# Performance work log

Hardware: AMD Instinct MI355X
Metric: run time of the kernel (lower is better)

Reference implementation:

```python
import jax, jax.numpy as jnp
import numpy as np

B, S, D = 1, 2048, 4096
NH, NKV, HD = 32, 8, 128
N_REP = NH // NKV
NEG = -1e9


def setup_inputs() -> dict:
    key = jax.random.key(0)
    ks = jax.random.split(key, 8)
    x = jax.random.normal(ks[0], (B, S, D), dtype=jnp.float32)
    # rotary freqs (theta=10000), shape [S, HD//2]
    inv = 1.0 / (10000.0 ** (jnp.arange(0, HD, 2, dtype=jnp.float32) / HD))
    ang = jnp.arange(S, dtype=jnp.float32)[:, None] * inv[None, :]
    freqs_cos, freqs_sin = jnp.cos(ang), jnp.sin(ang)
    # causal mask [1,1,S,S]
    row = jnp.arange(S)[:, None]
    col = jnp.arange(S)[None, :]
    mask = jnp.where(col <= row, 0.0, NEG).astype(jnp.float32)[None, None]
    input_indexes = jnp.arange(S, dtype=jnp.int64)
    cache_k = jnp.zeros((B, S, NKV, HD), dtype=jnp.float32)
    cache_v = jnp.zeros((B, S, NKV, HD), dtype=jnp.float32)
    sc = 0.02
    wq = jax.random.normal(ks[1], (NH * HD, D), dtype=jnp.float32) * sc
    wk = jax.random.normal(ks[2], (NKV * HD, D), dtype=jnp.float32) * sc
    wv = jax.random.normal(ks[3], (NKV * HD, D), dtype=jnp.float32) * sc
    wo = jax.random.normal(ks[4], (NH * HD, D), dtype=jnp.float32).T * sc
    return {"x": x, "freqs_cos": freqs_cos, "freqs_sin": freqs_sin, "mask": mask,
            "input_indexes": input_indexes, "cache_k": cache_k, "cache_v": cache_v,
            "wq": wq, "wk": wk, "wv": wv, "wo": wo}


def _rope(t, cos, sin):
    # t: [B,S,H,HD]; treat last dim as HD//2 complex pairs (even=real, odd=imag)
    tr = t.reshape(*t.shape[:-1], HD // 2, 2)
    xr, xi = tr[..., 0], tr[..., 1]
    c = cos[None, :, None, :]  # [1,S,1,HD//2]
    s = sin[None, :, None, :]
    outr = xr * c - xi * s
    outi = xr * s + xi * c
    return jnp.stack([outr, outi], axis=-1).reshape(t.shape)


def reference(x, freqs_cos, freqs_sin, mask, input_indexes, cache_k, cache_v, wq, wk, wv, wo):
    bsz, seqlen = x.shape[0], x.shape[-2]
    xq = (x @ wq.T).reshape(bsz, seqlen, NH, HD)
    xk = (x @ wk.T).reshape(bsz, seqlen, NKV, HD)
    xv = (x @ wv.T).reshape(bsz, seqlen, NKV, HD)
    xq = _rope(xq, freqs_cos, freqs_sin)
    xk = _rope(xk, freqs_cos, freqs_sin)
    # KV-cache append (index_copy along seq dim)
    cache_k = cache_k.at[:, input_indexes].set(xk)
    cache_v = cache_v.at[:, input_indexes].set(xv)
    # GQA: repeat kv heads
    keys = jnp.repeat(cache_k, N_REP, axis=2)    # [B,S,NH,HD]
    values = jnp.repeat(cache_v, N_REP, axis=2)
    scores = jnp.einsum('bshd,bthd->bhst', xq, keys) / jnp.sqrt(jnp.float32(HD))
    scores = scores + mask
    probs = jax.nn.softmax(scores.astype(jnp.float32), axis=-1).astype(xq.dtype)
    out = jnp.einsum('bhst,bthd->bhsd', probs, values)
    out = out.transpose(0, 2, 1, 3).reshape(bsz, seqlen, -1)
    return (out @ wo.T, cache_k, cache_v)
```

## Files before the change

kernel.cpp:

```cpp
#include <hip/hip_runtime.h>
#include <cstdint>

#define S_LEN 2048
#define D_DIM 4096
#define NH_ 32
#define NKV_ 8
#define HD_ 128
#define GK 4096

typedef unsigned short u16;
typedef __attribute__((ext_vector_type(4))) float f32x4;
typedef __attribute__((ext_vector_type(8))) short bf16x8;
typedef __attribute__((ext_vector_type(4))) short s16x4;

__device__ __forceinline__ short f2bf(float f) {
  union { float f; unsigned int u; } v; v.f = f;
  unsigned int r = v.u + 0x7fffu + ((v.u >> 16) & 1u);
  return (short)(r >> 16);
}

__device__ __forceinline__ void glds16(const void* g, void* l) {
  __builtin_amdgcn_global_load_lds(
      (const __attribute__((address_space(1))) void*)g,
      (__attribute__((address_space(3))) void*)l, 16, 0, 0);
}

__global__ __launch_bounds__(256) void cvt_bf16(const float* __restrict__ src,
                                                u16* __restrict__ dst, int n8) {
  int i = blockIdx.x * 256 + threadIdx.x;
  if (i < n8) {
    float4 a = *(const float4*)&src[(size_t)i * 8];
    float4 b = *(const float4*)&src[(size_t)i * 8 + 4];
    bf16x8 o = { f2bf(a.x), f2bf(a.y), f2bf(a.z), f2bf(a.w),
                 f2bf(b.x), f2bf(b.y), f2bf(b.z), f2bf(b.w) };
    *(bf16x8*)&dst[(size_t)i * 8] = o;
  }
}

template <int MODE>
__global__ __launch_bounds__(256) void gemm_bf(const u16* __restrict__ A,
                                               const u16* __restrict__ W,
                                               float* __restrict__ C,
                                               u16* __restrict__ qbf,
                                               u16* __restrict__ kbf,
                                               u16* __restrict__ vbf,
                                               float* __restrict__ cko,
                                               float* __restrict__ cvo,
                                               const float* __restrict__ fc,
                                               const float* __restrict__ fs,
                                               int N) {
  __shared__ __align__(16) u16 As[128 * 64];
  __shared__ __align__(16) u16 Bs[128 * 64];
  const int t = threadIdx.x;
  const int lane = t & 63;
  const int wave = t >> 6;
  const int wm = (wave >> 1) * 64;
  const int wn = (wave & 1) * 64;
  const int quad = lane >> 4;
  const int L = lane & 15;
  const int bm = blockIdx.y * 128;
  const int bn = blockIdx.x * 128;
  const int dr = lane >> 3;
  const int cb = lane & 7;
  const int cbs = cb ^ dr;

  f32x4 acc[4][4];
#pragma unroll
  for (int i = 0; i < 4; ++i)
#pragma unroll
    for (int j = 0; j < 4; ++j) { f32x4 z = {0.f, 0.f, 0.f, 0.f}; acc[i][j] = z; }

  for (int k0 = 0; k0 < GK; k0 += 64) {
    __syncthreads();
#pragma unroll
    for (int q = 0; q < 4; ++q) {
      int chunk = wave * 4 + q;
      int row = chunk * 8 + dr;
      glds16(&A[(size_t)(bm + row) * GK + k0 + cbs * 8], &As[chunk * 512]);
      glds16(&W[(size_t)(bn + row) * GK + k0 + cbs * 8], &Bs[chunk * 512]);
    }
    __syncthreads();
#pragma unroll
    for (int s = 0; s < 2; ++s) {
      bf16x8 af[4], bw[4];
#pragma unroll
      for (int i = 0; i < 4; ++i)
        af[i] = *(const bf16x8*)&As[(wm + 16 * i + L) * 64 + (((s * 4 + quad) ^ (L & 7)) * 8)];
#pragma unroll
      for (int j = 0; j < 4; ++j)
        bw[j] = *(const bf16x8*)&Bs[(wn + 16 * j + L) * 64 + (((s * 4 + quad) ^ (L & 7)) * 8)];
#pragma unroll
      for (int i = 0; i < 4; ++i)
#pragma unroll
        for (int j = 0; j < 4; ++j)
          acc[i][j] = __builtin_amdgcn_mfma_f32_16x16x32_bf16(af[i], bw[j], acc[i][j], 0, 0, 0);
    }
  }

  if (MODE == 0) {
#pragma unroll
    for (int i = 0; i < 4; ++i) {
      int r0 = bm + wm + i * 16 + quad * 4;
#pragma unroll
      for (int j = 0; j < 4; ++j) {
        int c = bn + wn + j * 16 + L;
#pragma unroll
        for (int r = 0; r < 4; ++r) C[(size_t)(r0 + r) * N + c] = acc[i][j][r];
      }
    }
  } else {
    const float scale = 0.08838834764831845f;
#pragma unroll
    for (int i = 0; i < 4; ++i) {
#pragma unroll
      for (int j = 0; j < 4; ++j) {
        int c = bn + wn + 16 * j + L;
#pragma unroll
        for (int r = 0; r < 4; ++r) {
          int srow = bm + wm + 16 * i + 4 * quad + r;
          float v = acc[i][j][r];
          float partner = __shfl_xor(v, 1);
          if (c < 4096) {
            int p = (c >> 1) & 63;
            float co = fc[srow * 64 + p], si = fs[srow * 64 + p];
            float out = (c & 1) ? partner * si + v * co : v * co - partner * si;
            qbf[(size_t)srow * 4096 + c] = (u16)f2bf(out * scale);
          } else if (c < 5120) {
            int p = (c >> 1) & 63;
            float co = fc[srow * 64 + p], si = fs[srow * 64 + p];
            float out = (c & 1) ? partner * si + v * co : v * co - partner * si;
            int cc = c - 4096;
            cko[(size_t)srow * 1024 + cc] = out;
            kbf[(size_t)srow * 1024 + cc] = (u16)f2bf(out);
          } else {
            int cc = c - 5120;
            cvo[(size_t)srow * 1024 + cc] = v;
            vbf[(size_t)srow * 1024 + cc] = (u16)f2bf(v);
          }
        }
      }
    }
  }
}

__global__ __launch_bounds__(256, 3) void attn_bf(const u16* __restrict__ qbf,
                                                  const u16* __restrict__ kbf,
                                                  const u16* __restrict__ vbf,
                                                  u16* __restrict__ ao) {
  __shared__ __align__(16) u16 Ks[64 * 136];
  __shared__ __align__(16) u16 Vt[128 * 64];
  __shared__ __align__(16) u16 Ps[4 * 16 * 72];
  const int t = threadIdx.x;
  const int wave = t >> 6;
  const int lane = t & 63;
  const int Q4 = lane >> 4;
  const int L = lane & 15;
  const int h = blockIdx.y;
  const int qb = 31 - (int)blockIdx.x;
  const int kvh = h >> 2;
  const int qs0 = qb * 64;
  u16* Psw = &Ps[wave * 16 * 72];

  bf16x8 qf[4];
  {
    const u16* qbase = &qbf[(size_t)(qs0 + 16 * wave + L) * D_DIM + h * HD_ + 8 * Q4];
#pragma unroll
    for (int s = 0; s < 4; ++s) qf[s] = *(const bf16x8*)&qbase[32 * s];
  }

  f32x4 o[8];
#pragma unroll
  for (int jd = 0; jd < 8; ++jd) { f32x4 z = {0.f, 0.f, 0.f, 0.f}; o[jd] = z; }
  float mold[4] = {-1e30f, -1e30f, -1e30f, -1e30f};
  float lst[4] = {0.f, 0.f, 0.f, 0.f};

  for (int kt = 0; kt <= qb; ++kt) {
    __syncthreads();
    const u16* kb = &kbf[(size_t)(kt * 64) * (NKV_ * HD_) + kvh * HD_];
    const u16* vb = &vbf[(size_t)(kt * 64) * (NKV_ * HD_) + kvh * HD_];
#pragma unroll
    for (int p = 0; p < 4; ++p) {
      int u = t + 256 * p;
      int r = u >> 4, c8 = u & 15;
      *(bf16x8*)&Ks[r * 136 + c8 * 8] =
          *(const bf16x8*)&kb[(size_t)r * (NKV_ * HD_) + c8 * 8];
    }
#pragma unroll
    for (int p = 0; p < 4; ++p) {
      int u = t + 256 * p;
      int d = u & 127, bb = u >> 7;
      const u16* vsrc = &vb[(size_t)(bb * 8) * (NKV_ * HD_) + d];
      short vv[8];
#pragma unroll
      for (int j = 0; j < 8; ++j) vv[j] = (short)vsrc[(size_t)j * (NKV_ * HD_)];
      bf16x8 pk = { vv[0], vv[1], vv[2], vv[3], vv[4], vv[5], vv[6], vv[7] };
      *(bf16x8*)&Vt[d * 64 + ((bb + d) & 7) * 8] = pk;
    }
    __syncthreads();

    f32x4 sa[4];
#pragma unroll
    for (int jn = 0; jn < 4; ++jn) { f32x4 z = {0.f, 0.f, 0.f, 0.f}; sa[jn] = z; }
#pragma unroll
    for (int s = 0; s < 4; ++s) {
#pragma unroll
      for (int jn = 0; jn < 4; ++jn) {
        bf16x8 kf = *(const bf16x8*)&Ks[(16 * jn + L) * 136 + 32 * s + 8 * Q4];
        sa[jn] = __builtin_amdgcn_mfma_f32_16x16x32_bf16(qf[s], kf, sa[jn], 0, 0, 0);
      }
    }

    const int gq0 = qs0 + 16 * wave + 4 * Q4;
    const int gk0 = kt * 64 + L;
    float rmax[4];
#pragma unroll
    for (int r = 0; r < 4; ++r) {
#pragma unroll
      for (int jn = 0; jn < 4; ++jn)
        if (gk0 + 16 * jn > gq0 + r) sa[jn][r] = -1e30f;
      rmax[r] = fmaxf(fmaxf(sa[0][r], sa[1][r]), fmaxf(sa[2][r], sa[3][r]));
    }
#pragma unroll
    for (int m = 1; m < 16; m <<= 1) {
#pragma unroll
      for (int r = 0; r < 4; ++r) rmax[r] = fmaxf(rmax[r], __shfl_xor(rmax[r], m));
    }
    float p_[4][4], rsum[4], alpha[4];
#pragma unroll
    for (int r = 0; r < 4; ++r) {
      float mnew = fmaxf(mold[r], rmax[r]);
      alpha[r] = __expf(mold[r] - mnew);
#pragma unroll
      for (int jn = 0; jn < 4; ++jn) p_[jn][r] = __expf(sa[jn][r] - mnew);
      rsum[r] = (p_[0][r] + p_[1][r]) + (p_[2][r] + p_[3][r]);
      mold[r] = mnew;
    }
#pragma unroll
    for (int m = 1; m < 16; m <<= 1) {
#pragma unroll
      for (int r = 0; r < 4; ++r) rsum[r] += __shfl_xor(rsum[r], m);
    }
#pragma unroll
    for (int r = 0; r < 4; ++r) lst[r] = lst[r] * alpha[r] + rsum[r];
#pragma unroll
    for (int jd = 0; jd < 8; ++jd)
#pragma unroll
      for (int r = 0; r < 4; ++r) o[jd][r] *= alpha[r];

#pragma unroll
    for (int r = 0; r < 4; ++r)
#pragma unroll
      for (int jn = 0; jn < 4; ++jn)
        Psw[(4 * Q4 + r) * 72 + 16 * jn + L] = (u16)f2bf(p_[jn][r]);
    asm volatile("s_waitcnt lgkmcnt(0)" ::: "memory");

#pragma unroll
    for (int s2 = 0; s2 < 2; ++s2) {
      bf16x8 pa = *(const bf16x8*)&Psw[L * 72 + 32 * s2 + 8 * Q4];
#pragma unroll
      for (int jd = 0; jd < 8; ++jd) {
        bf16x8 vf = *(const bf16x8*)&Vt[(16 * jd + L) * 64 + ((4 * s2 + Q4 + L) & 7) * 8];
        o[jd] = __builtin_amdgcn_mfma_f32_16x16x32_bf16(pa, vf, o[jd], 0, 0, 0);
      }
    }
  }

  float inv[4];
#pragma unroll
  for (int r = 0; r < 4; ++r) inv[r] = 1.0f / lst[r];
#pragma unroll
  for (int r = 0; r < 4; ++r) {
    u16* dst = &ao[(size_t)(qs0 + 16 * wave + 4 * Q4 + r) * D_DIM + h * HD_ + L];
#pragma unroll
    for (int jd = 0; jd < 8; ++jd) dst[16 * jd] = (u16)f2bf(o[jd][r] * inv[r]);
  }
}

#define LDA 40
__global__ __launch_bounds__(256) void gemm_bt(const float* __restrict__ A,
                                               const float* __restrict__ W,
                                               float* __restrict__ C, int N) {
  __shared__ short As[128 * LDA];
  __shared__ short Bs[128 * LDA];
  const int t = threadIdx.x;
  const int lane = t & 63;
  const int wave = t >> 6;
  const int wm = (wave >> 1) * 64;
  const int wn = (wave & 1) * 64;
  const int quad = lane >> 4;
  const int l15 = lane & 15;
  const int bm = blockIdx.y * 128;
  const int bn = blockIdx.x * 128;
  f32x4 acc[4][4];
#pragma unroll
  for (int i = 0; i < 4; ++i)
#pragma unroll
    for (int j = 0; j < 4; ++j) { f32x4 z = {0.f, 0.f, 0.f, 0.f}; acc[i][j] = z; }
  for (int k0 = 0; k0 < GK; k0 += 32) {
    __syncthreads();
#pragma unroll
    for (int p = 0; p < 4; ++p) {
      int idx = p * 256 + t;
      int row = idx >> 3;
      int c4 = (idx & 7) * 4;
      const float4 av = *(const float4*)&A[(size_t)(bm + row) * GK + k0 + c4];
      const float4 wv = *(const float4*)&W[(size_t)(bn + row) * GK + k0 + c4];
      s16x4 a4 = { f2bf(av.x), f2bf(av.y), f2bf(av.z), f2bf(av.w) };
      s16x4 w4 = { f2bf(wv.x), f2bf(wv.y), f2bf(wv.z), f2bf(wv.w) };
      *(s16x4*)&As[row * LDA + c4] = a4;
      *(s16x4*)&Bs[row * LDA + c4] = w4;
    }
    __syncthreads();
    bf16x8 af[4], bfr[4];
#pragma unroll
    for (int i = 0; i < 4; ++i) {
      af[i]  = *(const bf16x8*)&As[(wm + i * 16 + l15) * LDA + quad * 8];
      bfr[i] = *(const bf16x8*)&Bs[(wn + i * 16 + l15) * LDA + quad * 8];
    }
#pragma unroll
    for (int i = 0; i < 4; ++i)
#pragma unroll
      for (int j = 0; j < 4; ++j)
        acc[i][j] = __builtin_amdgcn_mfma_f32_16x16x32_bf16(af[i], bfr[j], acc[i][j], 0, 0, 0);
  }
#pragma unroll
  for (int i = 0; i < 4; ++i) {
    int r0 = bm + wm + i * 16 + quad * 4;
#pragma unroll
    for (int j = 0; j < 4; ++j) {
      int c = bn + wn + j * 16 + l15;
#pragma unroll
      for (int r = 0; r < 4; ++r) C[(size_t)(r0 + r) * N + c] = acc[i][j][r];
    }
  }
}

__global__ __launch_bounds__(256) void rope_kernel(float* __restrict__ xq,
                                                   const float* __restrict__ xk,
                                                   float* __restrict__ cko,
                                                   const float* __restrict__ fc,
                                                   const float* __restrict__ fs) {
  int i = blockIdx.x * 256 + threadIdx.x;
  const int NQP = S_LEN * NH_ * (HD_ / 2);
  if (i < NQP) {
    int s = i >> 11; int rem = i & 2047; int p = rem & 63;
    float c = fc[s * 64 + p], sn = fs[s * 64 + p];
    float2 v = *(const float2*)&xq[(size_t)s * D_DIM + 2 * rem];
    *(float2*)&xq[(size_t)s * D_DIM + 2 * rem] =
        make_float2(v.x * c - v.y * sn, v.x * sn + v.y * c);
  } else {
    int j = i - NQP; int s = j >> 9; int rem = j & 511; int p = rem & 63;
    float c = fc[s * 64 + p], sn = fs[s * 64 + p];
    float2 v = *(const float2*)&xk[(size_t)s * (NKV_ * HD_) + 2 * rem];
    *(float2*)&cko[(size_t)s * (NKV_ * HD_) + 2 * rem] =
        make_float2(v.x * c - v.y * sn, v.x * sn + v.y * c);
  }
}

__global__ __launch_bounds__(256, 3) void attn_mfma(const float* __restrict__ xq,
                                                    const float* __restrict__ ck,
                                                    const float* __restrict__ cv,
                                                    float* __restrict__ outp) {
  __shared__ __align__(16) short Ks[64 * 136];
  __shared__ __align__(16) short Vt[128 * 64];
  __shared__ __align__(16) short Ps[4 * 16 * 72];
  const int t = threadIdx.x;
  const int wave = t >> 6;
  const int lane = t & 63;
  const int Q4 = lane >> 4;
  const int L = lane & 15;
  const int h = blockIdx.y;
  const int qb = 31 - (int)blockIdx.x;
  const int kvh = h >> 2;
  const int qs0 = qb * 64;
  const float scale = 0.08838834764831845f;
  short* Psw = &Ps[wave * 16 * 72];
  bf16x8 qf[4];
  {
    const float* qbase = &xq[(size_t)(qs0 + 16 * wave + L) * D_DIM + h * HD_ + 8 * Q4];
#pragma unroll
    for (int s = 0; s < 4; ++s) {
      float4 a = *(const float4*)&qbase[32 * s];
      float4 b = *(const float4*)&qbase[32 * s + 4];
      bf16x8 q8 = { f2bf(a.x * scale), f2bf(a.y * scale), f2bf(a.z * scale), f2bf(a.w * scale),
                    f2bf(b.x * scale), f2bf(b.y * scale), f2bf(b.z * scale), f2bf(b.w * scale) };
      qf[s] = q8;
    }
  }
  f32x4 o[8];
#pragma unroll
  for (int jd = 0; jd < 8; ++jd) { f32x4 z = {0.f, 0.f, 0.f, 0.f}; o[jd] = z; }
  float mold[4] = {-1e30f, -1e30f, -1e30f, -1e30f};
  float lst[4] = {0.f, 0.f, 0.f, 0.f};
  for (int kt = 0; kt <= qb; ++kt) {
    __syncthreads();
    const float* ckb = &ck[(size_t)(kt * 64) * (NKV_ * HD_) + kvh * HD_];
    const float* cvb = &cv[(size_t)(kt * 64) * (NKV_ * HD_) + kvh * HD_];
#pragma unroll
    for (int p = 0; p < 8; ++p) {
      int i = t + 256 * p;
      int r = i >> 5, c4 = (i & 31) * 4;
      float4 v = *(const float4*)&ckb[(size_t)r * (NKV_ * HD_) + c4];
      s16x4 k4 = { f2bf(v.x), f2bf(v.y), f2bf(v.z), f2bf(v.w) };
      *(s16x4*)&Ks[r * 136 + c4] = k4;
    }
#pragma unroll
    for (int p = 0; p < 4; ++p) {
      int u = t + 256 * p;
      int d = u & 127, bb = u >> 7;
      float vv[8];
#pragma unroll
      for (int j = 0; j < 8; ++j) vv[j] = cvb[(size_t)(bb * 8 + j) * (NKV_ * HD_) + d];
      bf16x8 pk = { f2bf(vv[0]), f2bf(vv[1]), f2bf(vv[2]), f2bf(vv[3]),
                    f2bf(vv[4]), f2bf(vv[5]), f2bf(vv[6]), f2bf(vv[7]) };
      *(bf16x8*)&Vt[d * 64 + ((bb + d) & 7) * 8] = pk;
    }
    __syncthreads();
    f32x4 sa[4];
#pragma unroll
    for (int jn = 0; jn < 4; ++jn) { f32x4 z = {0.f, 0.f, 0.f, 0.f}; sa[jn] = z; }
#pragma unroll
    for (int s = 0; s < 4; ++s) {
#pragma unroll
      for (int jn = 0; jn < 4; ++jn) {
        bf16x8 kf = *(const bf16x8*)&Ks[(16 * jn + L) * 136 + 32 * s + 8 * Q4];
        sa[jn] = __builtin_amdgcn_mfma_f32_16x16x32_bf16(qf[s], kf, sa[jn], 0, 0, 0);
      }
    }
    const int gq0 = qs0 + 16 * wave + 4 * Q4;
    const int gk0 = kt * 64 + L;
    float rmax[4];
#pragma unroll
    for (int r = 0; r < 4; ++r) {
#pragma unroll
      for (int jn = 0; jn < 4; ++jn)
        if (gk0 + 16 * jn > gq0 + r) sa[jn][r] = -1e30f;
      rmax[r] = fmaxf(fmaxf(sa[0][r], sa[1][r]), fmaxf(sa[2][r], sa[3][r]));
    }
#pragma unroll
    for (int m = 1; m < 16; m <<= 1) {
#pragma unroll
      for (int r = 0; r < 4; ++r) rmax[r] = fmaxf(rmax[r], __shfl_xor(rmax[r], m));
    }
    float p_[4][4], rsum[4], alpha[4];
#pragma unroll
    for (int r = 0; r < 4; ++r) {
      float mnew = fmaxf(mold[r], rmax[r]);
      alpha[r] = __expf(mold[r] - mnew);
#pragma unroll
      for (int jn = 0; jn < 4; ++jn) p_[jn][r] = __expf(sa[jn][r] - mnew);
      rsum[r] = (p_[0][r] + p_[1][r]) + (p_[2][r] + p_[3][r]);
      mold[r] = mnew;
    }
#pragma unroll
    for (int m = 1; m < 16; m <<= 1) {
#pragma unroll
      for (int r = 0; r < 4; ++r) rsum[r] += __shfl_xor(rsum[r], m);
    }
#pragma unroll
    for (int r = 0; r < 4; ++r) lst[r] = lst[r] * alpha[r] + rsum[r];
#pragma unroll
    for (int jd = 0; jd < 8; ++jd)
#pragma unroll
      for (int r = 0; r < 4; ++r) o[jd][r] *= alpha[r];
#pragma unroll
    for (int r = 0; r < 4; ++r)
#pragma unroll
      for (int jn = 0; jn < 4; ++jn)
        Psw[(4 * Q4 + r) * 72 + 16 * jn + L] = f2bf(p_[jn][r]);
    asm volatile("s_waitcnt lgkmcnt(0)" ::: "memory");
#pragma unroll
    for (int s2 = 0; s2 < 2; ++s2) {
      bf16x8 pa = *(const bf16x8*)&Psw[L * 72 + 32 * s2 + 8 * Q4];
#pragma unroll
      for (int jd = 0; jd < 8; ++jd) {
        bf16x8 vf = *(const bf16x8*)&Vt[(16 * jd + L) * 64 + ((4 * s2 + Q4 + L) & 7) * 8];
        o[jd] = __builtin_amdgcn_mfma_f32_16x16x32_bf16(pa, vf, o[jd], 0, 0, 0);
      }
    }
  }
  float inv[4];
#pragma unroll
  for (int r = 0; r < 4; ++r) inv[r] = 1.0f / lst[r];
#pragma unroll
  for (int r = 0; r < 4; ++r) {
    float* dst = &outp[(size_t)(qs0 + 16 * wave + 4 * Q4 + r) * D_DIM + h * HD_ + L];
#pragma unroll
    for (int jd = 0; jd < 8; ++jd) dst[16 * jd] = o[jd][r] * inv[r];
  }
}

extern "C" void kernel_launch(void* const* d_in, const int* in_sizes, int n_in,
                              void* d_out, int out_size, void* d_ws, size_t ws_size,
                              hipStream_t stream) {
  (void)in_sizes; (void)n_in; (void)out_size;
  const float* x  = (const float*)d_in[0];
  const float* fc = (const float*)d_in[1];
  const float* fs = (const float*)d_in[2];
  const float* wq = (const float*)d_in[7];
  const float* wk = (const float*)d_in[8];
  const float* wv = (const float*)d_in[9];
  const float* wo = (const float*)d_in[10];
  float* outp = (float*)d_out;
  float* ck = outp + (size_t)S_LEN * D_DIM;
  float* cv = ck + (size_t)S_LEN * NKV_ * HD_;

  if (ws_size >= 109051904ull) {
    u16* x_bf = (u16*)d_ws;
    u16* wqkv = x_bf + 8388608;
    u16* q_bf = wqkv + 25165824;
    u16* k_bf = q_bf + 8388608;
    u16* v_bf = k_bf + 2097152;
    u16* ao_bf = v_bf + 2097152;
    u16* wo_bf = wqkv;

    cvt_bf16<<<4096, 256, 0, stream>>>(x, x_bf, 1048576);
    cvt_bf16<<<8192, 256, 0, stream>>>(wq, wqkv, 2097152);
    cvt_bf16<<<2048, 256, 0, stream>>>(wk, wqkv + 16777216, 524288);
    cvt_bf16<<<2048, 256, 0, stream>>>(wv, wqkv + 20971520, 524288);
    gemm_bf<1><<<dim3(48, 16), 256, 0, stream>>>(x_bf, wqkv, nullptr, q_bf,
                                                 k_bf, v_bf, ck, cv, fc, fs, 6144);
    cvt_bf16<<<8192, 256, 0, stream>>>(wo, wo_bf, 2097152);
    attn_bf<<<dim3(32, 32), 256, 0, stream>>>(q_bf, k_bf, v_bf, ao_bf);
    gemm_bf<0><<<dim3(32, 16), 256, 0, stream>>>(ao_bf, wo_bf, outp, nullptr,
                                                 nullptr, nullptr, nullptr,
                                                 nullptr, fc, fs, 4096);
  } else {
    float* xq = (float*)d_ws;
    float* xk = xq + (size_t)S_LEN * D_DIM;
    dim3 blk(256);
    gemm_bt<<<dim3(32, 16), blk, 0, stream>>>(x, wq, xq, 4096);
    gemm_bt<<<dim3(8, 16),  blk, 0, stream>>>(x, wk, xk, 1024);
    gemm_bt<<<dim3(8, 16),  blk, 0, stream>>>(x, wv, cv, 1024);
    rope_kernel<<<20480, 256, 0, stream>>>(xq, xk, ck, fc, fs);
    attn_mfma<<<dim3(32, 32), 512 / 2, 0, stream>>>(xq, ck, cv, xq);
    gemm_bt<<<dim3(32, 16), blk, 0, stream>>>(xq, wo, outp, 4096);
  }
}
```

Baseline: 650.6 us.

## Replace bf16 GEMM with 256x256 tile, 8-wave, double-buffered pipelined kernel

Swaps the 128x128 single-buffered GEMM for a 256x256 tile kernel with 8 waves and double-buffered LDS. Global-to-LDS loads are issued in quarter stages and interleaved with MFMA phases, with explicit vmcnt and lgkmcnt waits, barriers and priority raises. The goal is to hide load latency and raise operand reuse per block. In exchange the grid gets much smaller (192 and 128 blocks on 256 CUs), so some CUs may sit idle, and register pressure rises.

```diff
diff --git a/kernel.cpp b/kernel.cpp
--- a/kernel.cpp
+++ b/kernel.cpp
@@ -38,87 +38,173 @@
 }
 
 template <int MODE>
-__global__ __launch_bounds__(256) void gemm_bf(const u16* __restrict__ A,
-                                               const u16* __restrict__ W,
-                                               float* __restrict__ C,
-                                               u16* __restrict__ qbf,
-                                               u16* __restrict__ kbf,
-                                               u16* __restrict__ vbf,
-                                               float* __restrict__ cko,
-                                               float* __restrict__ cvo,
-                                               const float* __restrict__ fc,
-                                               const float* __restrict__ fs,
-                                               int N) {
-  __shared__ __align__(16) u16 As[128 * 64];
-  __shared__ __align__(16) u16 Bs[128 * 64];
+__global__ __launch_bounds__(512, 1) void gemm8(const u16* __restrict__ Amat,
+                                                const u16* __restrict__ W,
+                                                float* __restrict__ C,
+                                                u16* __restrict__ qbf,
+                                                u16* __restrict__ kbf,
+                                                u16* __restrict__ vbf,
+                                                float* __restrict__ cko,
+                                                float* __restrict__ cvo,
+                                                const float* __restrict__ fc,
+                                                const float* __restrict__ fs,
+                                                int N) {
+  __shared__ __align__(16) u16 As[2][16384];
+  __shared__ __align__(16) u16 Bs[2][16384];
   const int t = threadIdx.x;
   const int lane = t & 63;
   const int wave = t >> 6;
-  const int wm = (wave >> 1) * 64;
-  const int wn = (wave & 1) * 64;
+  const int wr = wave >> 2;
+  const int wc = wave & 3;
   const int quad = lane >> 4;
   const int L = lane & 15;
-  const int bm = blockIdx.y * 128;
-  const int bn = blockIdx.x * 128;
+  const int bm = blockIdx.y * 256;
+  const int bn = blockIdx.x * 256;
   const int dr = lane >> 3;
   const int cb = lane & 7;
   const int cbs = cb ^ dr;
-
-  f32x4 acc[4][4];
-#pragma unroll
-  for (int i = 0; i < 4; ++i)
+  const int NT = GK / 64;
+
+  auto stage = [&](int s) {
+    const int tile = s >> 2;
+    const int p = s & 3;
+    const int half = p & 1;
+    const int buf = tile & 1;
+    const int k0 = tile << 6;
+    const bool isB = (p < 2);
+    const u16* src = isB ? W : Amat;
+    const int base = isB ? bn : bm;
+    u16* dst = isB ? &Bs[buf][0] : &As[buf][0];
+    const int chunk0 = half * 16 + wave * 2;
+#pragma unroll
+    for (int c = 0; c < 2; ++c) {
+      const int chunk = chunk0 + c;
+      const int row = chunk * 8 + dr;
+      glds16(&src[(size_t)(base + row) * GK + k0 + cbs * 8], &dst[chunk * 512]);
+    }
+  };
+
+  f32x4 acc[8][4];
+#pragma unroll
+  for (int i = 0; i < 8; ++i)
 #pragma unroll
     for (int j = 0; j < 4; ++j) { f32x4 z = {0.f, 0.f, 0.f, 0.f}; acc[i][j] = z; }
 
-  for (int k0 = 0; k0 < GK; k0 += 64) {
-    __syncthreads();
-#pragma unroll
-    for (int q = 0; q < 4; ++q) {
-      int chunk = wave * 4 + q;
-      int row = chunk * 8 + dr;
-      glds16(&A[(size_t)(bm + row) * GK + k0 + cbs * 8], &As[chunk * 512]);
-      glds16(&W[(size_t)(bn + row) * GK + k0 + cbs * 8], &Bs[chunk * 512]);
-    }
-    __syncthreads();
-#pragma unroll
-    for (int s = 0; s < 2; ++s) {
-      bf16x8 af[4], bw[4];
-#pragma unroll
-      for (int i = 0; i < 4; ++i)
-        af[i] = *(const bf16x8*)&As[(wm + 16 * i + L) * 64 + (((s * 4 + quad) ^ (L & 7)) * 8)];
-#pragma unroll
-      for (int j = 0; j < 4; ++j)
-        bw[j] = *(const bf16x8*)&Bs[(wn + 16 * j + L) * 64 + (((s * 4 + quad) ^ (L & 7)) * 8)];
-#pragma unroll
-      for (int i = 0; i < 4; ++i)
-#pragma unroll
-        for (int j = 0; j < 4; ++j)
-          acc[i][j] = __builtin_amdgcn_mfma_f32_16x16x32_bf16(af[i], bw[j], acc[i][j], 0, 0, 0);
-    }
+  stage(0); stage(1); stage(2); stage(3);
+  asm volatile("s_waitcnt vmcnt(4)" ::: "memory");
+  stage(4); stage(5); stage(6);
+  asm volatile("s_waitcnt vmcnt(6)" ::: "memory");
+  __builtin_amdgcn_s_barrier();
+  __builtin_amdgcn_sched_barrier(0);
+
+  bf16x8 af[4][2], bw[4][2];
+  const int arow = wr * 128;
+  const int brow = wc * 64;
+
+  for (int kt = 0; kt < NT; ++kt) {
+    const u16* as = &As[kt & 1][0];
+    const u16* bs = &Bs[kt & 1][0];
+#pragma unroll
+    for (int i = 0; i < 4; ++i)
+#pragma unroll
+      for (int k = 0; k < 2; ++k)
+        af[i][k] = *(const bf16x8*)&as[(arow + i * 16 + L) * 64 +
+                                       (((k * 4 + quad) ^ (L & 7)) * 8)];
+#pragma unroll
+    for (int j = 0; j < 4; ++j)
+#pragma unroll
+      for (int k = 0; k < 2; ++k)
+        bw[j][k] = *(const bf16x8*)&bs[(brow + j * 16 + L) * 64 +
+                                       (((k * 4 + quad) ^ (L & 7)) * 8)];
+    { int s = 4 * kt + 7; if (s < 4 * NT) stage(s); }
+    __builtin_amdgcn_s_barrier();
+    asm volatile("s_waitcnt lgkmcnt(0)" ::: "memory");
+    __builtin_amdgcn_sched_barrier(0);
+    __builtin_amdgcn_s_setprio(1);
+#pragma unroll
+    for (int i = 0; i < 4; ++i)
+#pragma unroll
+      for (int j = 0; j < 2; ++j)
+#pragma unroll
+        for (int k = 0; k < 2; ++k)
+          acc[i][j] = __builtin_amdgcn_mfma_f32_16x16x32_bf16(af[i][k], bw[j][k],
+                                                              acc[i][j], 0, 0, 0);
+    __builtin_amdgcn_s_setprio(0);
+    __builtin_amdgcn_s_barrier();
+    { int s = 4 * kt + 8; if (s < 4 * NT) stage(s); }
+    __builtin_amdgcn_s_barrier();
+    __builtin_amdgcn_s_setprio(1);
+#pragma unroll
+    for (int i = 0; i < 4; ++i)
+#pragma unroll
+      for (int j = 0; j < 2; ++j)
+#pragma unroll
+        for (int k = 0; k < 2; ++k)
+          acc[i][2 + j] = __builtin_amdgcn_mfma_f32_16x16x32_bf16(
+              af[i][k], bw[2 + j][k], acc[i][2 + j], 0, 0, 0);
+    __builtin_amdgcn_s_setprio(0);
+    __builtin_amdgcn_s_barrier();
+#pragma unroll
+    for (int i = 0; i < 4; ++i)
+#pragma unroll
+      for (int k = 0; k < 2; ++k)
+        af[i][k] = *(const bf16x8*)&as[(arow + 64 + i * 16 + L) * 64 +
+                                       (((k * 4 + quad) ^ (L & 7)) * 8)];
+    { int s = 4 * kt + 9; if (s < 4 * NT) stage(s); }
+    __builtin_amdgcn_s_barrier();
+    asm volatile("s_waitcnt lgkmcnt(0)" ::: "memory");
+    __builtin_amdgcn_sched_barrier(0);
+    __builtin_amdgcn_s_setprio(1);
+#pragma unroll
+    for (int i = 0; i < 4; ++i)
+#pragma unroll
+      for (int j = 0; j < 2; ++j)
+#pragma unroll
+        for (int k = 0; k < 2; ++k)
+          acc[4 + i][j] = __builtin_amdgcn_mfma_f32_16x16x32_bf16(
+              af[i][k], bw[j][k], acc[4 + i][j], 0, 0, 0);
+    __builtin_amdgcn_s_setprio(0);
+    __builtin_amdgcn_s_barrier();
+    { int s = 4 * kt + 10; if (s < 4 * NT) stage(s); }
+    __builtin_amdgcn_s_barrier();
+    __builtin_amdgcn_s_setprio(1);
+#pragma unroll
+    for (int i = 0; i < 4; ++i)
+#pragma unroll
+      for (int j = 0; j < 2; ++j)
+#pragma unroll
+        for (int k = 0; k < 2; ++k)
+          acc[4 + i][2 + j] = __builtin_amdgcn_mfma_f32_16x16x32_bf16(
+              af[i][k], bw[2 + j][k], acc[4 + i][2 + j], 0, 0, 0);
+    __builtin_amdgcn_s_setprio(0);
+    if (kt + 2 < NT) asm volatile("s_waitcnt vmcnt(6)" ::: "memory");
+    else             asm volatile("s_waitcnt vmcnt(0)" ::: "memory");
+    __builtin_amdgcn_s_barrier();
+    __builtin_amdgcn_sched_barrier(0);
   }
 
   if (MODE == 0) {
 #pragma unroll
-    for (int i = 0; i < 4; ++i) {
-      int r0 = bm + wm + i * 16 + quad * 4;
-#pragma unroll
-      for (int j = 0; j < 4; ++j) {
-        int c = bn + wn + j * 16 + L;
-#pragma unroll
-        for (int r = 0; r < 4; ++r) C[(size_t)(r0 + r) * N + c] = acc[i][j][r];
+    for (int mi = 0; mi < 8; ++mi) {
+      int r0 = bm + wr * 128 + mi * 16 + quad * 4;
+#pragma unroll
+      for (int ni = 0; ni < 4; ++ni) {
+        int c = bn + wc * 64 + ni * 16 + L;
+#pragma unroll
+        for (int r = 0; r < 4; ++r) C[(size_t)(r0 + r) * N + c] = acc[mi][ni][r];
       }
     }
   } else {
     const float scale = 0.08838834764831845f;
 #pragma unroll
-    for (int i = 0; i < 4; ++i) {
-#pragma unroll
-      for (int j = 0; j < 4; ++j) {
-        int c = bn + wn + 16 * j + L;
+    for (int mi = 0; mi < 8; ++mi) {
+#pragma unroll
+      for (int ni = 0; ni < 4; ++ni) {
+        int c = bn + wc * 64 + ni * 16 + L;
 #pragma unroll
         for (int r = 0; r < 4; ++r) {
-          int srow = bm + wm + 16 * i + 4 * quad + r;
-          float v = acc[i][j][r];
+          int srow = bm + wr * 128 + mi * 16 + 4 * quad + r;
+          float v = acc[mi][ni][r];
           float partner = __shfl_xor(v, 1);
           if (c < 4096) {
             int p = (c >> 1) & 63;
@@ -518,13 +604,13 @@
     cvt_bf16<<<8192, 256, 0, stream>>>(wq, wqkv, 2097152);
     cvt_bf16<<<2048, 256, 0, stream>>>(wk, wqkv + 16777216, 524288);
     cvt_bf16<<<2048, 256, 0, stream>>>(wv, wqkv + 20971520, 524288);
-    gemm_bf<1><<<dim3(48, 16), 256, 0, stream>>>(x_bf, wqkv, nullptr, q_bf,
-                                                 k_bf, v_bf, ck, cv, fc, fs, 6144);
+    gemm8<1><<<dim3(24, 8), 512, 0, stream>>>(x_bf, wqkv, nullptr, q_bf,
+                                              k_bf, v_bf, ck, cv, fc, fs, 6144);
     cvt_bf16<<<8192, 256, 0, stream>>>(wo, wo_bf, 2097152);
     attn_bf<<<dim3(32, 32), 256, 0, stream>>>(q_bf, k_bf, v_bf, ao_bf);
-    gemm_bf<0><<<dim3(32, 16), 256, 0, stream>>>(ao_bf, wo_bf, outp, nullptr,
-                                                 nullptr, nullptr, nullptr,
-                                                 nullptr, fc, fs, 4096);
+    gemm8<0><<<dim3(16, 8), 512, 0, stream>>>(ao_bf, wo_bf, outp, nullptr,
+                                              nullptr, nullptr, nullptr,
+                                              nullptr, fc, fs, 4096);
   } else {
     float* xq = (float*)d_ws;
     float* xk = xq + (size_t)S_LEN * D_DIM;
```

Result: slower. 684.4 us (+5.2%).

## Use 256x256 double-buffered GEMM tiles and 128-row attention blocks

Applied to the files above, without the earlier changes.

Replaces the 128x128 bf16 GEMM with a 512-thread kernel that computes 256x256 output tiles. It double-buffers LDS with staggered A/B prefetch, manual waitcnt/barrier scheduling and s_setprio around the MFMA bursts. The attention kernel moves to 512 threads handling 128 query rows per block, which halves redundant K/V tile loads per head. The larger tiles shrink the grids (192 and 128 GEMM blocks, 512 attention blocks), which may leave compute units idle on a large GPU. The attention change also relies on the unshown causal-masking code handling the new tile count.

```diff
diff --git a/kernel.cpp b/kernel.cpp
--- a/kernel.cpp
+++ b/kernel.cpp
@@ -38,87 +38,130 @@
 }
 
 template <int MODE>
-__global__ __launch_bounds__(256) void gemm_bf(const u16* __restrict__ A,
-                                               const u16* __restrict__ W,
-                                               float* __restrict__ C,
-                                               u16* __restrict__ qbf,
-                                               u16* __restrict__ kbf,
-                                               u16* __restrict__ vbf,
-                                               float* __restrict__ cko,
-                                               float* __restrict__ cvo,
-                                               const float* __restrict__ fc,
-                                               const float* __restrict__ fs,
-                                               int N) {
-  __shared__ __align__(16) u16 As[128 * 64];
-  __shared__ __align__(16) u16 Bs[128 * 64];
+__global__ __launch_bounds__(512, 2) void gemm8(const u16* __restrict__ Amat,
+                                                const u16* __restrict__ W,
+                                                float* __restrict__ C,
+                                                u16* __restrict__ qbf,
+                                                u16* __restrict__ kbf,
+                                                u16* __restrict__ vbf,
+                                                float* __restrict__ cko,
+                                                float* __restrict__ cvo,
+                                                const float* __restrict__ fc,
+                                                const float* __restrict__ fs,
+                                                int N) {
+  __shared__ __align__(16) u16 As[2][16384];
+  __shared__ __align__(16) u16 Bs[2][16384];
   const int t = threadIdx.x;
   const int lane = t & 63;
   const int wave = t >> 6;
-  const int wm = (wave >> 1) * 64;
-  const int wn = (wave & 1) * 64;
+  const int wr = wave >> 2;
+  const int wc = wave & 3;
   const int quad = lane >> 4;
   const int L = lane & 15;
-  const int bm = blockIdx.y * 128;
-  const int bn = blockIdx.x * 128;
+  const int bm = blockIdx.y * 256;
+  const int bn = blockIdx.x * 256;
   const int dr = lane >> 3;
   const int cb = lane & 7;
   const int cbs = cb ^ dr;
-
-  f32x4 acc[4][4];
-#pragma unroll
-  for (int i = 0; i < 4; ++i)
+  const int NT = GK / 64;
+
+  auto stageA = [&](int tile) {
+    u16* dst = &As[tile & 1][0];
+    const int k0 = tile << 6;
+#pragma unroll
+    for (int c = 0; c < 4; ++c) {
+      const int chunk = wave * 4 + c;
+      const int row = chunk * 8 + dr;
+      glds16(&Amat[(size_t)(bm + row) * GK + k0 + cbs * 8], &dst[chunk * 512]);
+    }
+  };
+  auto stageB = [&](int tile) {
+    u16* dst = &Bs[tile & 1][0];
+    const int k0 = tile << 6;
+#pragma unroll
+    for (int c = 0; c < 4; ++c) {
+      const int chunk = wave * 4 + c;
+      const int row = chunk * 8 + dr;
+      glds16(&W[(size_t)(bn + row) * GK + k0 + cbs * 8], &dst[chunk * 512]);
+    }
+  };
+
+  f32x4 acc[8][4];
+#pragma unroll
+  for (int i = 0; i < 8; ++i)
 #pragma unroll
     for (int j = 0; j < 4; ++j) { f32x4 z = {0.f, 0.f, 0.f, 0.f}; acc[i][j] = z; }
 
-  for (int k0 = 0; k0 < GK; k0 += 64) {
-    __syncthreads();
-#pragma unroll
-    for (int q = 0; q < 4; ++q) {
-      int chunk = wave * 4 + q;
-      int row = chunk * 8 + dr;
-      glds16(&A[(size_t)(bm + row) * GK + k0 + cbs * 8], &As[chunk * 512]);
-      glds16(&W[(size_t)(bn + row) * GK + k0 + cbs * 8], &Bs[chunk * 512]);
-    }
-    __syncthreads();
-#pragma unroll
-    for (int s = 0; s < 2; ++s) {
-      bf16x8 af[4], bw[4];
+  stageB(0); stageA(0); stageB(1);
+  asm volatile("s_waitcnt vmcnt(4)" ::: "memory");
+  __builtin_amdgcn_s_barrier();
+  __builtin_amdgcn_sched_barrier(0);
+
+  bf16x8 af[4], bw[4];
+  const int arow = wr * 128;
+  const int brow = wc * 64;
+
+  for (int kt = 0; kt < NT; ++kt) {
+    const u16* as = &As[kt & 1][0];
+    const u16* bs = &Bs[kt & 1][0];
+#pragma unroll
+    for (int ph = 0; ph < 4; ++ph) {
+      const int mh = ph & 1;
+      const int s = ph >> 1;
 #pragma unroll
       for (int i = 0; i < 4; ++i)
-        af[i] = *(const bf16x8*)&As[(wm + 16 * i + L) * 64 + (((s * 4 + quad) ^ (L & 7)) * 8)];
-#pragma unroll
-      for (int j = 0; j < 4; ++j)
-        bw[j] = *(const bf16x8*)&Bs[(wn + 16 * j + L) * 64 + (((s * 4 + quad) ^ (L & 7)) * 8)];
+        af[i] = *(const bf16x8*)&as[(arow + mh * 64 + i * 16 + L) * 64 +
+                                     (((s * 4 + quad) ^ (L & 7)) * 8)];
+      if (ph == 0 || ph == 2) {
+#pragma unroll
+        for (int j = 0; j < 4; ++j)
+          bw[j] = *(const bf16x8*)&bs[(brow + j * 16 + L) * 64 +
+                                       (((s * 4 + quad) ^ (L & 7)) * 8)];
+      }
+      if (ph == 0 && kt + 1 < NT) stageA(kt + 1);
+      if (ph == 3 && kt + 2 < NT) stageB(kt + 2);
+      __builtin_amdgcn_s_barrier();
+      asm volatile("s_waitcnt lgkmcnt(0)" ::: "memory");
+      __builtin_amdgcn_sched_barrier(0);
+      __builtin_amdgcn_s_setprio(1);
 #pragma unroll
       for (int i = 0; i < 4; ++i)
 #pragma unroll
         for (int j = 0; j < 4; ++j)
-          acc[i][j] = __builtin_amdgcn_mfma_f32_16x16x32_bf16(af[i], bw[j], acc[i][j], 0, 0, 0);
+          acc[mh * 4 + i][j] = __builtin_amdgcn_mfma_f32_16x16x32_bf16(
+              af[i], bw[j], acc[mh * 4 + i][j], 0, 0, 0);
+      __builtin_amdgcn_s_setprio(0);
+      if (ph == 3) {
+        if (kt + 2 < NT) asm volatile("s_waitcnt vmcnt(4)" ::: "memory");
+        else             asm volatile("s_waitcnt vmcnt(0)" ::: "memory");
+      }
+      __builtin_amdgcn_s_barrier();
+      __builtin_amdgcn_sched_barrier(0);
     }
   }
 
   if (MODE == 0) {
 #pragma unroll
-    for (int i = 0; i < 4; ++i) {
-      int r0 = bm + wm + i * 16 + quad * 4;
-#pragma unroll
-      for (int j = 0; j < 4; ++j) {
-        int c = bn + wn + j * 16 + L;
-#pragma unroll
-        for (int r = 0; r < 4; ++r) C[(size_t)(r0 + r) * N + c] = acc[i][j][r];
+    for (int mi = 0; mi < 8; ++mi) {
+      int r0 = bm + wr * 128 + mi * 16 + quad * 4;
+#pragma unroll
+      for (int ni = 0; ni < 4; ++ni) {
+        int c = bn + wc * 64 + ni * 16 + L;
+#pragma unroll
+        for (int r = 0; r < 4; ++r) C[(size_t)(r0 + r) * N + c] = acc[mi][ni][r];
       }
     }
   } else {
     const float scale = 0.08838834764831845f;
 #pragma unroll
-    for (int i = 0; i < 4; ++i) {
-#pragma unroll
-      for (int j = 0; j < 4; ++j) {
-        int c = bn + wn + 16 * j + L;
+    for (int mi = 0; mi < 8; ++mi) {
+#pragma unroll
+      for (int ni = 0; ni < 4; ++ni) {
+        int c = bn + wc * 64 + ni * 16 + L;
 #pragma unroll
         for (int r = 0; r < 4; ++r) {
-          int srow = bm + wm + 16 * i + 4 * quad + r;
-          float v = acc[i][j][r];
+          int srow = bm + wr * 128 + mi * 16 + 4 * quad + r;
+          float v = acc[mi][ni][r];
           float partner = __shfl_xor(v, 1);
           if (c < 4096) {
             int p = (c >> 1) & 63;
@@ -143,22 +186,22 @@
   }
 }
 
-__global__ __launch_bounds__(256, 3) void attn_bf(const u16* __restrict__ qbf,
+__global__ __launch_bounds__(512, 2) void attn_bf(const u16* __restrict__ qbf,
                                                   const u16* __restrict__ kbf,
                                                   const u16* __restrict__ vbf,
                                                   u16* __restrict__ ao) {
   __shared__ __align__(16) u16 Ks[64 * 136];
   __shared__ __align__(16) u16 Vt[128 * 64];
-  __shared__ __align__(16) u16 Ps[4 * 16 * 72];
+  __shared__ __align__(16) u16 Ps[8 * 16 * 72];
   const int t = threadIdx.x;
   const int wave = t >> 6;
   const int lane = t & 63;
   const int Q4 = lane >> 4;
   const int L = lane & 15;
   const int h = blockIdx.y;
-  const int qb = 31 - (int)blockIdx.x;
+  const int qb = 15 - (int)blockIdx.x;
   const int kvh = h >> 2;
-  const int qs0 = qb * 64;
+  const int qs0 = qb * 128;
   u16* Psw = &Ps[wave * 16 * 72];
 
   bf16x8 qf[4];
@@ -174,20 +217,21 @@
   float mold[4] = {-1e30f, -1e30f, -1e30f, -1e30f};
   float lst[4] = {0.f, 0.f, 0.f, 0.f};
 
-  for (int kt = 0; kt <= qb; ++kt) {
+  const int NKT = 2 * qb + 2;
+  for (int kt = 0; kt < NKT; ++kt) {
     __syncthreads();
     const u16* kb = &kbf[(size_t)(kt * 64) * (NKV_ * HD_) + kvh * HD_];
     const u16* vb = &vbf[(size_t)(kt * 64) * (NKV_ * HD_) + kvh * HD_];
 #pragma unroll
-    for (int p = 0; p < 4; ++p) {
-      int u = t + 256 * p;
+    for (int p = 0; p < 2; ++p) {
+      int u = t + 512 * p;
       int r = u >> 4, c8 = u & 15;
       *(bf16x8*)&Ks[r * 136 + c8 * 8] =
           *(const bf16x8*)&kb[(size_t)r * (NKV_ * HD_) + c8 * 8];
     }
 #pragma unroll
-    for (int p = 0; p < 4; ++p) {
-      int u = t + 256 * p;
+    for (int p = 0; p < 2; ++p) {
+      int u = t + 512 * p;
       int d = u & 127, bb = u >> 7;
       const u16* vsrc = &vb[(size_t)(bb * 8) * (NKV_ * HD_) + d];
       short vv[8];
@@ -518,13 +562,13 @@
     cvt_bf16<<<8192, 256, 0, stream>>>(wq, wqkv, 2097152);
     cvt_bf16<<<2048, 256, 0, stream>>>(wk, wqkv + 16777216, 524288);
     cvt_bf16<<<2048, 256, 0, stream>>>(wv, wqkv + 20971520, 524288);
-    gemm_bf<1><<<dim3(48, 16), 256, 0, stream>>>(x_bf, wqkv, nullptr, q_bf,
-                                                 k_bf, v_bf, ck, cv, fc, fs, 6144);
+    gemm8<1><<<dim3(24, 8), 512, 0, stream>>>(x_bf, wqkv, nullptr, q_bf,
+                                              k_bf, v_bf, ck, cv, fc, fs, 6144);
     cvt_bf16<<<8192, 256, 0, stream>>>(wo, wo_bf, 2097152);
-    attn_bf<<<dim3(32, 32), 256, 0, stream>>>(q_bf, k_bf, v_bf, ao_bf);
-    gemm_bf<0><<<dim3(32, 16), 256, 0, stream>>>(ao_bf, wo_bf, outp, nullptr,
-                                                 nullptr, nullptr, nullptr,
-                                                 nullptr, fc, fs, 4096);
+    attn_bf<<<dim3(16, 32), 512, 0, stream>>>(q_bf, k_bf, v_bf, ao_bf);
+    gemm8<0><<<dim3(16, 8), 512, 0, stream>>>(ao_bf, wo_bf, outp, nullptr,
+                                              nullptr, nullptr, nullptr,
+                                              nullptr, fc, fs, 4096);
   } else {
     float* xq = (float*)d_ws;
     float* xk = xq + (size_t)S_LEN * D_DIM;
```

After: 646.1 us. About the same (-0.7%).
